# Kernel optimization log

Measured on AMD Instinct MI355X. Metric: run time of the kernel, lower is better.

Reference implementation:

```python
import jax, jax.numpy as jnp
import numpy as np

NTOKENS = 8192
TOPK = 2
HIDDEN = 4096
NUM_GROUPS = 2
M_FULL = NTOKENS * TOPK


def setup_inputs() -> dict:
    key = jax.random.key(0)
    k1, k2 = jax.random.split(key)
    gemm_buffer = jax.random.normal(k1, (NUM_GROUPS, M_FULL, HIDDEN), dtype=jnp.float32)
    scatter_index = jax.random.randint(k2, (NTOKENS, TOPK), 0, M_FULL, dtype=jnp.int64)
    return {"gemm_buffer": gemm_buffer, "scatter_index": scatter_index}


def reference(gemm_buffer, scatter_index):
    # gemm_buffer: [G, M_full, N] partial GEMM outputs (G = num_groups)
    # scatter_index: [T, K] row indices into the permuted expert GEMM output
    # Per kernel: out[t] = sum_g sum_k gemm_buffer[g, scatter_index[t, k], :],
    # accumulated in fp32 then cast back to the buffer dtype.
    gathered = gemm_buffer[:, scatter_index, :]          # [G, T, K, N]
    out = gathered.astype(jnp.float32).sum(axis=(0, 2))  # [T, N]
    return out.astype(gemm_buffer.dtype)
```

## Files before the change

kernel.cpp:

```cpp
#include <hip/hip_runtime.h>

#define NTOKENS    8192
#define TOPK       2
#define HIDDEN     4096
#define NUM_GROUPS 2
#define M_FULL     (NTOKENS * TOPK)
#define H4         (HIDDEN / 4)

__global__ __launch_bounds__(256) void topk_gather_rs_kernel(
    const float4* __restrict__ buf,
    const int*    __restrict__ idx,
    float4*       __restrict__ out)
{
    const int t   = blockIdx.x;
    const int tid = threadIdx.x;

    const int r0 = idx[t * TOPK + 0];
    const int r1 = idx[t * TOPK + 1];

    const size_t g1off = (size_t)M_FULL * H4;

    const float4* __restrict__ p00 = buf + (size_t)r0 * H4;
    const float4* __restrict__ p01 = buf + (size_t)r1 * H4;
    const float4* __restrict__ p10 = buf + g1off + (size_t)r0 * H4;
    const float4* __restrict__ p11 = buf + g1off + (size_t)r1 * H4;

    float4* __restrict__ o = out + (size_t)t * H4;

#pragma unroll
    for (int j = 0; j < H4 / 256; ++j) {
        const int c = j * 256 + tid;
        const float4 a = p00[c];
        const float4 b = p01[c];
        const float4 cc = p10[c];
        const float4 d = p11[c];
        float4 s;
        s.x = (a.x + b.x) + (cc.x + d.x);
        s.y = (a.y + b.y) + (cc.y + d.y);
        s.z = (a.z + b.z) + (cc.z + d.z);
        s.w = (a.w + b.w) + (cc.w + d.w);
        o[c] = s;
    }
}

extern "C" void kernel_launch(void* const* d_in, const int* in_sizes, int n_in,
                              void* d_out, int out_size, void* d_ws, size_t ws_size,
                              hipStream_t stream) {
    const float4* buf = (const float4*)d_in[0];
    const int*    idx = (const int*)d_in[1];
    float4*       out = (float4*)d_out;

    topk_gather_rs_kernel<<<NTOKENS, 256, 0, stream>>>(buf, idx, out);
}
```

Measured before the change: 691.7 us.

## Use persistent grid-stride blocks with index prefetch, staggered loads, nontemporal stores

Launches a fixed grid of 2048 blocks that loop over tokens and prefetch the next token's scatter indices while processing the current one. The four source rows are read in a rotated chunk order so the concurrent streams hit different offsets, and results accumulate in registers. Output is written with nontemporal stores to avoid polluting cache. The cost is more registers per thread for the accumulator array and the rotated order changes fp32 summation order.

```diff
diff --git a/kernel.cpp b/kernel.cpp
--- a/kernel.cpp
+++ b/kernel.cpp
@@ -6,49 +6,79 @@
 #define NUM_GROUPS 2
 #define M_FULL     (NTOKENS * TOPK)
 #define H4         (HIDDEN / 4)
+#define TPB        256
+#define NBLOCKS    2048
+#define CHUNK      (H4 / TPB)
 
-__global__ __launch_bounds__(256) void topk_gather_rs_kernel(
-    const float4* __restrict__ buf,
-    const int*    __restrict__ idx,
-    float4*       __restrict__ out)
+typedef float f32x4 __attribute__((ext_vector_type(4)));
+
+__global__ __launch_bounds__(TPB) void topk_gather_rs_kernel(
+    const f32x4* __restrict__ buf,
+    const int*   __restrict__ idx,
+    f32x4*       __restrict__ out)
 {
-    const int t   = blockIdx.x;
     const int tid = threadIdx.x;
-
-    const int r0 = idx[t * TOPK + 0];
-    const int r1 = idx[t * TOPK + 1];
-
     const size_t g1off = (size_t)M_FULL * H4;
 
-    const float4* __restrict__ p00 = buf + (size_t)r0 * H4;
-    const float4* __restrict__ p01 = buf + (size_t)r1 * H4;
-    const float4* __restrict__ p10 = buf + g1off + (size_t)r0 * H4;
-    const float4* __restrict__ p11 = buf + g1off + (size_t)r1 * H4;
+    int t = blockIdx.x;
+    int r0 = idx[t * TOPK + 0];
+    int r1 = idx[t * TOPK + 1];
 
-    float4* __restrict__ o = out + (size_t)t * H4;
+    while (t < NTOKENS) {
+        const int nt = t + NBLOCKS;
+        int nr0 = 0, nr1 = 0;
+        if (nt < NTOKENS) {
+            nr0 = idx[nt * TOPK + 0];
+            nr1 = idx[nt * TOPK + 1];
+        }
+
+        const f32x4* __restrict__ p00 = buf + (size_t)r0 * H4;
+        const f32x4* __restrict__ p01 = buf + (size_t)r1 * H4;
+        const f32x4* __restrict__ p10 = buf + g1off + (size_t)r0 * H4;
+        const f32x4* __restrict__ p11 = buf + g1off + (size_t)r1 * H4;
+        f32x4* __restrict__ o = out + (size_t)t * H4;
+
+        f32x4 acc[CHUNK];
+#pragma unroll
+        for (int j = 0; j < CHUNK; ++j) {
+            acc[j] = (f32x4)(0.f);
+        }
 
 #pragma unroll
-    for (int j = 0; j < H4 / 256; ++j) {
-        const int c = j * 256 + tid;
-        const float4 a = p00[c];
-        const float4 b = p01[c];
-        const float4 cc = p10[c];
-        const float4 d = p11[c];
-        float4 s;
-        s.x = (a.x + b.x) + (cc.x + d.x);
-        s.y = (a.y + b.y) + (cc.y + d.y);
-        s.z = (a.z + b.z) + (cc.z + d.z);
-        s.w = (a.w + b.w) + (cc.w + d.w);
-        o[c] = s;
+        for (int j = 0; j < CHUNK; ++j) {
+            const int k0 = (j + 0) & (CHUNK - 1);
+            const int k1 = (j + 1) & (CHUNK - 1);
+            const int k2 = (j + 2) & (CHUNK - 1);
+            const int k3 = (j + 3) & (CHUNK - 1);
+
+            const f32x4 a = p00[k0 * TPB + tid];
+            const f32x4 b = p01[k1 * TPB + tid];
+            const f32x4 c = p10[k2 * TPB + tid];
+            const f32x4 d = p11[k3 * TPB + tid];
+
+            acc[k0] += a;
+            acc[k1] += b;
+            acc[k2] += c;
+            acc[k3] += d;
+        }
+
+#pragma unroll
+        for (int j = 0; j < CHUNK; ++j) {
+            __builtin_nontemporal_store(acc[j], &o[j * TPB + tid]);
+        }
+
+        t  = nt;
+        r0 = nr0;
+        r1 = nr1;
     }
 }
 
 extern "C" void kernel_launch(void* const* d_in, const int* in_sizes, int n_in,
                               void* d_out, int out_size, void* d_ws, size_t ws_size,
                               hipStream_t stream) {
-    const float4* buf = (const float4*)d_in[0];
-    const int*    idx = (const int*)d_in[1];
-    float4*       out = (float4*)d_out;
+    const f32x4* buf = (const f32x4*)d_in[0];
+    const int*   idx = (const int*)d_in[1];
+    f32x4*       out = (f32x4*)d_out;
 
-    topk_gather_rs_kernel<<<NTOKENS, 256, 0, stream>>>(buf, idx, out);
+    topk_gather_rs_kernel<<<NBLOCKS, TPB, 0, stream>>>(buf, idx, out);
 }
```

After: 695.2 us. No clear change (+0.5%).
